# Optimization experiments

Hardware: AMD Instinct MI355X
Metric: run time of the kernel (lower is better)

The kernel has to match this reference:

```python
import jax, jax.numpy as jnp
import numpy as np

D = 2048  # input_size
H = 2048  # hidden_size
K = 4096  # number of children


def setup_inputs() -> dict:
    key = jax.random.key(0)
    ks = jax.random.split(key, 12)
    sD = 1.0 / np.sqrt(D)
    sH = 1.0 / np.sqrt(H)
    return {
        "input": jax.random.normal(ks[0], (D,), dtype=jnp.float32),
        "children_c": jax.random.normal(ks[1], (K, H), dtype=jnp.float32),
        "children_h": jax.random.normal(ks[2], (K, H), dtype=jnp.float32),
        "W_iou_x": jax.random.uniform(ks[3], (3 * H, D), jnp.float32, -sD, sD),
        "b_iou_x": jax.random.uniform(ks[4], (3 * H,), jnp.float32, -sD, sD),
        "W_iou_h": jax.random.uniform(ks[5], (3 * H, H), jnp.float32, -sH, sH),
        "b_iou_h": jax.random.uniform(ks[6], (3 * H,), jnp.float32, -sH, sH),
        "W_fx": jax.random.uniform(ks[7], (H, D), jnp.float32, -sD, sD),
        "b_fx": jax.random.uniform(ks[8], (H,), jnp.float32, -sD, sD),
        "W_fh": jax.random.uniform(ks[9], (H, H), jnp.float32, -sH, sH),
        "b_fh": jax.random.uniform(ks[10], (H,), jnp.float32, -sH, sH),
    }


def reference(input, children_c, children_h,
              W_iou_x, b_iou_x, W_iou_h, b_iou_h,
              W_fx, b_fx, W_fh, b_fh):
    # iou = iou_x(input) + iou_h(sum_k h_k)  -> [3H]
    h_sum = jnp.sum(children_h, axis=0)
    iou = (W_iou_x @ input + b_iou_x) + (W_iou_h @ h_sum + b_iou_h)
    i, o, u = jnp.split(iou, 3)
    i = jax.nn.sigmoid(i)
    o = jax.nn.sigmoid(o)
    u = jnp.tanh(u)
    # per-child forget gates, batched over K (original loops in Python):
    # f_k = sigmoid(f_x(input) + f_h(h_k))  -> [K, H]
    fx = W_fx @ input + b_fx                       # [H], computed once
    fh = children_h @ W_fh.T + b_fh                # [K, H] GEMM
    f = jax.nn.sigmoid(fx[None, :] + fh)           # [K, H]
    c = i * u + jnp.sum(f * children_c, axis=0)    # [H]
    h = o * jnp.tanh(c)                            # [H]
    return (o, c, h)
```

## Files before the change

### kernel.cpp

```cpp
#include <hip/hip_runtime.h>

typedef unsigned short u16;
typedef short bf16x8 __attribute__((ext_vector_type(8)));
typedef float f32x4 __attribute__((ext_vector_type(4)));

#define D_IN 2048
#define H_DIM 2048
#define K_CH 4096

__device__ __forceinline__ u16 f2bf(float f) {
  unsigned int u = __float_as_uint(f);
  u += 0x7fffu + ((u >> 16) & 1u);
  return (u16)(u >> 16);
}
__device__ __forceinline__ float sigmoidf(float x) {
  return 1.0f / (1.0f + __expf(-x));
}
__device__ __forceinline__ uint4 packrow(float4 a, float4 b) {
  uint4 w;
  w.x = (unsigned)f2bf(a.x) | ((unsigned)f2bf(a.y) << 16);
  w.y = (unsigned)f2bf(a.z) | ((unsigned)f2bf(a.w) << 16);
  w.z = (unsigned)f2bf(b.x) | ((unsigned)f2bf(b.y) << 16);
  w.w = (unsigned)f2bf(b.z) | ((unsigned)f2bf(b.w) << 16);
  return w;
}

__global__ __launch_bounds__(256) void k1(
    const float* __restrict__ ch, const float* __restrict__ wfh,
    const float* __restrict__ Wfx, const float* __restrict__ bfx,
    const float* __restrict__ bfh, const float* __restrict__ x,
    const float* __restrict__ Wix, const float* __restrict__ bix,
    const float* __restrict__ bih, float* __restrict__ partials,
    u16* __restrict__ chb, u16* __restrict__ wfhb, float* __restrict__ g,
    float* __restrict__ ioux, float* __restrict__ hsum,
    float* __restrict__ accv) {
  const int t = threadIdx.x;
  const int bid = blockIdx.x;
  if (bid < 1024) {
    const int r0 = bid * 4;
    float4 a[4], b[4];
#pragma unroll
    for (int r = 0; r < 4; ++r) {
      const float4* p = (const float4*)(ch + (size_t)(r0 + r) * H_DIM + t * 8);
      a[r] = p[0];
      b[r] = p[1];
    }
    float s0 = 0.f, s1 = 0.f, s2 = 0.f, s3 = 0.f;
    float s4 = 0.f, s5 = 0.f, s6 = 0.f, s7 = 0.f;
#pragma unroll
    for (int r = 0; r < 4; ++r) {
      s0 += a[r].x; s1 += a[r].y; s2 += a[r].z; s3 += a[r].w;
      s4 += b[r].x; s5 += b[r].y; s6 += b[r].z; s7 += b[r].w;
      *(uint4*)(chb + (size_t)(r0 + r) * H_DIM + t * 8) = packrow(a[r], b[r]);
    }
    float4 lo, hi;
    lo.x = s0; lo.y = s1; lo.z = s2; lo.w = s3;
    hi.x = s4; hi.y = s5; hi.z = s6; hi.w = s7;
    float* pp = partials + (size_t)bid * H_DIM + t * 8;
    *(float4*)pp = lo;
    *(float4*)(pp + 4) = hi;
  } else if (bid < 1536) {
    const size_t base = (size_t)(bid - 1024) * 8192 + t * 8;
    float4 a[4], b[4];
#pragma unroll
    for (int j = 0; j < 4; ++j) {
      const float4* p = (const float4*)(wfh + base + j * 2048);
      a[j] = p[0];
      b[j] = p[1];
    }
#pragma unroll
    for (int j = 0; j < 4; ++j)
      *(uint4*)(wfhb + base + j * 2048) = packrow(a[j], b[j]);
  } else if (bid < 2048) {
    const int wave = t >> 6, lane = t & 63;
    const int h = (bid - 1536) * 4 + wave;
    const float4* w = (const float4*)(Wfx + (size_t)h * D_IN);
    const float4* xv = (const float4*)x;
    float s = 0.f;
#pragma unroll
    for (int i = 0; i < 8; ++i) {
      int idx = i * 64 + lane;
      float4 av = w[idx], bv = xv[idx];
      s += av.x * bv.x + av.y * bv.y + av.z * bv.z + av.w * bv.w;
    }
#pragma unroll
    for (int off = 32; off > 0; off >>= 1) s += __shfl_xor(s, off);
    if (lane == 0) g[h] = s + bfx[h] + bfh[h];
  } else if (bid < 3584) {
    const int wave = t >> 6, lane = t & 63;
    const int row = (bid - 2048) * 4 + wave;
    const float4* w = (const float4*)(Wix + (size_t)row * D_IN);
    const float4* xv = (const float4*)x;
    float s = 0.f;
#pragma unroll
    for (int i = 0; i < 8; ++i) {
      int idx = i * 64 + lane;
      float4 av = w[idx], bv = xv[idx];
      s += av.x * bv.x + av.y * bv.y + av.z * bv.z + av.w * bv.w;
    }
#pragma unroll
    for (int off = 32; off > 0; off >>= 1) s += __shfl_xor(s, off);
    if (lane == 0) ioux[row] = s + bix[row] + bih[row];
  } else {
    float4 z = {0.f, 0.f, 0.f, 0.f};
    ((float4*)hsum)[t * 2] = z;
    ((float4*)hsum)[t * 2 + 1] = z;
    ((float4*)accv)[t * 2] = z;
    ((float4*)accv)[t * 2 + 1] = z;
  }
}

#define BM 256
#define BN 128
#define BK 64

__global__ __launch_bounds__(512) void kG(
    const u16* __restrict__ chb, const float* __restrict__ cc,
    const u16* __restrict__ wfhb, const float* __restrict__ g,
    const float* __restrict__ partials, float* __restrict__ hsum,
    float* __restrict__ accv) {
  __shared__ u16 As[3][BM * BK];
  __shared__ u16 Bs[3][BN * BK];

  const int bid = blockIdx.x;
  const int t = threadIdx.x;

  if (bid < 64) {
    const int c = (bid & 7) * 256 + (t & 255);
    const int p0 = (bid >> 3) * 128 + (t >> 8) * 64;
    float a0 = 0.f, a1 = 0.f, a2 = 0.f, a3 = 0.f;
    float a4 = 0.f, a5 = 0.f, a6 = 0.f, a7 = 0.f;
    for (int p = p0; p < p0 + 64; p += 8) {
      a0 += partials[(size_t)(p + 0) * H_DIM + c];
      a1 += partials[(size_t)(p + 1) * H_DIM + c];
      a2 += partials[(size_t)(p + 2) * H_DIM + c];
      a3 += partials[(size_t)(p + 3) * H_DIM + c];
      a4 += partials[(size_t)(p + 4) * H_DIM + c];
      a5 += partials[(size_t)(p + 5) * H_DIM + c];
      a6 += partials[(size_t)(p + 6) * H_DIM + c];
      a7 += partials[(size_t)(p + 7) * H_DIM + c];
    }
    float s = ((a0 + a1) + (a2 + a3)) + ((a4 + a5) + (a6 + a7));
    atomicAdd(hsum + c, s);
    return;
  }

  const int gb = bid - 64;
  const int xcd = gb & 7;
  const int u = gb >> 3;
  const int bm = (xcd << 1) | (u >> 4);
  const int bn = u & 15;
  const int row0 = bm * BM;
  const int col0 = bn * BN;

  const int wave = t >> 6, lane = t & 63;
  const int lrow = lane & 15, lquad = lane >> 4;
  const int wm = wave >> 1, wn = wave & 1;

  f32x4 acc[4][4] = {};
  bf16x8 faA[2][4], fbA[2][4];
  bf16x8 faB[2][4], fbB[2][4];

  const int srow = lane >> 3;
  const int schunk = (lane & 7) ^ srow;
  const u16* agbase = chb  + (size_t)(row0 + wave * 32 + srow) * H_DIM + schunk * 8;
  const u16* bgbase = wfhb + (size_t)(col0 + wave * 16 + srow) * H_DIM + schunk * 8;

#define STAGE(bi, kb)                                                         \
  do {                                                                        \
    _Pragma("unroll")                                                         \
    for (int i = 0; i < 4; ++i)                                               \
      __builtin_amdgcn_global_load_lds(                                       \
          (const __attribute__((address_space(1))) void*)(agbase + (size_t)i * 8 * H_DIM + (size_t)(kb) * BK), \
          (__attribute__((address_space(3))) void*)(&As[bi][(wave * 32 + i * 8) * 64]), \
          16, 0, 0);                                                          \
    _Pragma("unroll")                                                         \
    for (int i = 0; i < 2; ++i)                                               \
      __builtin_amdgcn_global_load_lds(                                       \
          (const __attribute__((address_space(1))) void*)(bgbase + (size_t)i * 8 * H_DIM + (size_t)(kb) * BK), \
          (__attribute__((address_space(3))) void*)(&Bs[bi][(wave * 16 + i * 8) * 64]), \
          16, 0, 0);                                                          \
  } while (0)

#define READ_SET(fax, fbx, bi)                                                \
  do {                                                                        \
    _Pragma("unroll")                                                         \
    for (int step = 0; step < 2; ++step) {                                    \
      const int slot = ((step * 4 + lquad) ^ (lrow & 7)) * 8;                 \
      _Pragma("unroll")                                                       \
      for (int i = 0; i < 4; ++i)                                             \
        fax[step][i] = *(const bf16x8*)(&As[bi][(wm * 64 + i * 16 + lrow) * 64 + slot]); \
      _Pragma("unroll")                                                       \
      for (int i = 0; i < 4; ++i)                                             \
        fbx[step][i] = *(const bf16x8*)(&Bs[bi][(wn * 64 + i * 16 + lrow) * 64 + slot]); \
    }                                                                         \
  } while (0)

#define COMPUTE_SET(fax, fbx)                                                 \
  do {                                                                        \
    __builtin_amdgcn_s_setprio(1);                                            \
    _Pragma("unroll")                                                         \
    for (int step = 0; step < 2; ++step)                                      \
      _Pragma("unroll")                                                       \
      for (int mi = 0; mi < 4; ++mi)                                          \
        _Pragma("unroll")                                                     \
        for (int ni = 0; ni < 4; ++ni)                                        \
          acc[mi][ni] = __builtin_amdgcn_mfma_f32_16x16x32_bf16(              \
              fax[step][mi], fbx[step][ni], acc[mi][ni], 0, 0, 0);            \
    __builtin_amdgcn_s_setprio(0);                                            \
  } while (0)

#define VMCNT6() do { asm volatile("s_waitcnt vmcnt(6)" ::: "memory");        \
                      __builtin_amdgcn_sched_barrier(0); } while (0)
#define VMCNT0() do { asm volatile("s_waitcnt vmcnt(0)" ::: "memory");        \
                      __builtin_amdgcn_sched_barrier(0); } while (0)
#define LGKM15() do { asm volatile("s_waitcnt lgkmcnt(15)" ::: "memory");     \
                      __builtin_amdgcn_sched_barrier(0); } while (0)
#define LGKM0()  do { asm volatile("s_waitcnt lgkmcnt(0)" ::: "memory");      \
                      __builtin_amdgcn_sched_barrier(0); } while (0)
#define SBAR()   do { __builtin_amdgcn_s_barrier();                           \
                      __builtin_amdgcn_sched_barrier(0); } while (0)

  STAGE(0, 0);
  STAGE(1, 1);
  VMCNT6();
  SBAR();
  READ_SET(faA, fbA, 0);

  int c0 = 0, c1 = 1, c2 = 2;
  for (int kb = 0; kb < 30; kb += 2) {
    STAGE(c2, kb + 2);
    VMCNT6();
    SBAR();
    READ_SET(faB, fbB, c1);
    LGKM15();
    COMPUTE_SET(faA, fbA);
    SBAR();
    STAGE(c0, kb + 3);
    VMCNT6();
    SBAR();
    READ_SET(faA, fbA, c2);
    LGKM15();
    COMPUTE_SET(faB, fbB);
    SBAR();
    const int tmp = c0; c0 = c2; c2 = c1; c1 = tmp;
  }
  VMCNT0();
  SBAR();
  READ_SET(faB, fbB, 1);
  LGKM15();
  COMPUTE_SET(faA, fbA);
  LGKM0();
  COMPUTE_SET(faB, fbB);

#pragma unroll
  for (int ni = 0; ni < 4; ++ni) {
    const int colg = col0 + wn * 64 + ni * 16 + lrow;
    const float gv = g[colg];
    float s = 0.f;
#pragma unroll
    for (int mi = 0; mi < 4; ++mi) {
      const int rowg = row0 + wm * 64 + mi * 16 + lquad * 4;
#pragma unroll
      for (int r = 0; r < 4; ++r) {
        float f = sigmoidf(gv + acc[mi][ni][r]);
        s += f * cc[(size_t)(rowg + r) * H_DIM + colg];
      }
    }
    s += __shfl_xor(s, 16);
    s += __shfl_xor(s, 32);
    if (lquad == 0) atomicAdd(accv + colg, s);
  }
#undef STAGE
#undef READ_SET
#undef COMPUTE_SET
#undef VMCNT6
#undef VMCNT0
#undef LGKM15
#undef LGKM0
#undef SBAR
}

__global__ __launch_bounds__(256) void kmvF(const float* __restrict__ Wih,
                                            const float* __restrict__ hsum,
                                            const float* __restrict__ ioux,
                                            const float* __restrict__ accv,
                                            float* __restrict__ out) {
  const int wave = threadIdx.x >> 6, lane = threadIdx.x & 63;
  const int h = blockIdx.x * 4 + wave;
  const float4* w0 = (const float4*)(Wih + (size_t)h * H_DIM);
  const float4* w1 = (const float4*)(Wih + (size_t)(H_DIM + h) * H_DIM);
  const float4* w2 = (const float4*)(Wih + (size_t)(2 * H_DIM + h) * H_DIM);
  const float4* hv = (const float4*)hsum;
  float s0 = 0.f, s1 = 0.f, s2 = 0.f;
#pragma unroll
  for (int i = 0; i < 8; ++i) {
    int idx = i * 64 + lane;
    float4 b = hv[idx];
    float4 a0 = w0[idx], a1 = w1[idx], a2 = w2[idx];
    s0 += a0.x * b.x + a0.y * b.y + a0.z * b.z + a0.w * b.w;
    s1 += a1.x * b.x + a1.y * b.y + a1.z * b.z + a1.w * b.w;
    s2 += a2.x * b.x + a2.y * b.y + a2.z * b.z + a2.w * b.w;
  }
#pragma unroll
  for (int off = 32; off > 0; off >>= 1) {
    s0 += __shfl_xor(s0, off);
    s1 += __shfl_xor(s1, off);
    s2 += __shfl_xor(s2, off);
  }
  if (lane == 0) {
    float i_ = sigmoidf(ioux[h] + s0);
    float o_ = sigmoidf(ioux[H_DIM + h] + s1);
    float u_ = tanhf(ioux[2 * H_DIM + h] + s2);
    float c_ = i_ * u_ + accv[h];
    float hh = o_ * tanhf(c_);
    out[h] = o_;
    out[H_DIM + h] = c_;
    out[2 * H_DIM + h] = hh;
  }
}

extern "C" void kernel_launch(void* const* d_in, const int* in_sizes, int n_in,
                              void* d_out, int out_size, void* d_ws, size_t ws_size,
                              hipStream_t stream) {
  const float* x   = (const float*)d_in[0];
  const float* cc  = (const float*)d_in[1];
  const float* ch  = (const float*)d_in[2];
  const float* Wix = (const float*)d_in[3];
  const float* bix = (const float*)d_in[4];
  const float* Wih = (const float*)d_in[5];
  const float* bih = (const float*)d_in[6];
  const float* Wfx = (const float*)d_in[7];
  const float* bfx = (const float*)d_in[8];
  const float* Wfh = (const float*)d_in[9];
  const float* bfh = (const float*)d_in[10];

  float* ws   = (float*)d_ws;
  float* hsum = ws;
  float* ioux = ws + 2048;
  float* g    = ws + 8192;
  float* accv = ws + 10240;
  float* partials = ws + 12288;
  u16* chb  = (u16*)(ws + 12288 + 1024 * 2048);
  u16* wfhb = chb + (size_t)K_CH * H_DIM;
  float* out = (float*)d_out;

  k1<<<3585, 256, 0, stream>>>(ch, Wfh, Wfx, bfx, bfh, x, Wix, bix, bih,
                               partials, chb, wfhb, g, ioux, hsum, accv);
  kG<<<320, 512, 0, stream>>>(chb, cc, wfhb, g, partials, hsum, accv);
  kmvF<<<512, 256, 0, stream>>>(Wih, hsum, ioux, accv, out);
}
```

Measured before the change: 256.0 us.

## Restructure GEMM main loop into four-phase interleaved LDS-read/MFMA schedule

```diff
diff --git a/kernel.cpp b/kernel.cpp
--- a/kernel.cpp
+++ b/kernel.cpp
@@ -158,22 +158,39 @@
   const int wm = wave >> 1, wn = wave & 1;
 
   f32x4 acc[4][4] = {};
-  bf16x8 faA[2][4], fbA[2][4];
-  bf16x8 faB[2][4], fbB[2][4];
+  bf16x8 fa0[4], fb0[4], fa1[4], fb1[4];
 
   const int srow = lane >> 3;
   const int schunk = (lane & 7) ^ srow;
   const u16* agbase = chb  + (size_t)(row0 + wave * 32 + srow) * H_DIM + schunk * 8;
   const u16* bgbase = wfhb + (size_t)(col0 + wave * 16 + srow) * H_DIM + schunk * 8;
 
-#define STAGE(bi, kb)                                                         \
+  const int slot0 = ((lquad) ^ (lrow & 7)) * 8;
+  const int slot1 = ((4 + lquad) ^ (lrow & 7)) * 8;
+  const int arow0 = (wm * 64 + 0 * 16 + lrow) * 64;
+  const int arow1 = (wm * 64 + 1 * 16 + lrow) * 64;
+  const int arow2 = (wm * 64 + 2 * 16 + lrow) * 64;
+  const int arow3 = (wm * 64 + 3 * 16 + lrow) * 64;
+  const int brow0 = (wn * 64 + 0 * 16 + lrow) * 64;
+  const int brow1 = (wn * 64 + 1 * 16 + lrow) * 64;
+  const int brow2 = (wn * 64 + 2 * 16 + lrow) * 64;
+  const int brow3 = (wn * 64 + 3 * 16 + lrow) * 64;
+
+#define LDA(bi, roff, sl) (*(const bf16x8*)(&As[bi][(roff) + (sl)]))
+#define LDB(bi, roff, sl) (*(const bf16x8*)(&Bs[bi][(roff) + (sl)]))
+
+#define STAGE_A2(bi, kb, i0)                                                  \
   do {                                                                        \
     _Pragma("unroll")                                                         \
-    for (int i = 0; i < 4; ++i)                                               \
+    for (int i = (i0); i < (i0) + 2; ++i)                                     \
       __builtin_amdgcn_global_load_lds(                                       \
           (const __attribute__((address_space(1))) void*)(agbase + (size_t)i * 8 * H_DIM + (size_t)(kb) * BK), \
           (__attribute__((address_space(3))) void*)(&As[bi][(wave * 32 + i * 8) * 64]), \
           16, 0, 0);                                                          \
+  } while (0)
+
+#define STAGE_B2(bi, kb)                                                      \
+  do {                                                                        \
     _Pragma("unroll")                                                         \
     for (int i = 0; i < 2; ++i)                                               \
       __builtin_amdgcn_global_load_lds(                                       \
@@ -182,76 +199,72 @@
           16, 0, 0);                                                          \
   } while (0)
 
-#define READ_SET(fax, fbx, bi)                                                \
-  do {                                                                        \
-    _Pragma("unroll")                                                         \
-    for (int step = 0; step < 2; ++step) {                                    \
-      const int slot = ((step * 4 + lquad) ^ (lrow & 7)) * 8;                 \
-      _Pragma("unroll")                                                       \
-      for (int i = 0; i < 4; ++i)                                             \
-        fax[step][i] = *(const bf16x8*)(&As[bi][(wm * 64 + i * 16 + lrow) * 64 + slot]); \
-      _Pragma("unroll")                                                       \
-      for (int i = 0; i < 4; ++i)                                             \
-        fbx[step][i] = *(const bf16x8*)(&Bs[bi][(wn * 64 + i * 16 + lrow) * 64 + slot]); \
-    }                                                                         \
-  } while (0)
-
-#define COMPUTE_SET(fax, fbx)                                                 \
+#define MFMA_HALF(fa, fb, M0)                                                 \
   do {                                                                        \
     __builtin_amdgcn_s_setprio(1);                                            \
     _Pragma("unroll")                                                         \
-    for (int step = 0; step < 2; ++step)                                      \
+    for (int mi = (M0); mi < (M0) + 2; ++mi)                                  \
       _Pragma("unroll")                                                       \
-      for (int mi = 0; mi < 4; ++mi)                                          \
-        _Pragma("unroll")                                                     \
-        for (int ni = 0; ni < 4; ++ni)                                        \
-          acc[mi][ni] = __builtin_amdgcn_mfma_f32_16x16x32_bf16(              \
-              fax[step][mi], fbx[step][ni], acc[mi][ni], 0, 0, 0);            \
+      for (int ni = 0; ni < 4; ++ni)                                          \
+        acc[mi][ni] = __builtin_amdgcn_mfma_f32_16x16x32_bf16(                \
+            fa[mi], fb[ni], acc[mi][ni], 0, 0, 0);                            \
     __builtin_amdgcn_s_setprio(0);                                            \
   } while (0)
 
 #define VMCNT6() do { asm volatile("s_waitcnt vmcnt(6)" ::: "memory");        \
                       __builtin_amdgcn_sched_barrier(0); } while (0)
 #define VMCNT0() do { asm volatile("s_waitcnt vmcnt(0)" ::: "memory");        \
-                      __builtin_amdgcn_sched_barrier(0); } while (0)
-#define LGKM15() do { asm volatile("s_waitcnt lgkmcnt(15)" ::: "memory");     \
                       __builtin_amdgcn_sched_barrier(0); } while (0)
 #define LGKM0()  do { asm volatile("s_waitcnt lgkmcnt(0)" ::: "memory");      \
                       __builtin_amdgcn_sched_barrier(0); } while (0)
 #define SBAR()   do { __builtin_amdgcn_s_barrier();                           \
                       __builtin_amdgcn_sched_barrier(0); } while (0)
 
-  STAGE(0, 0);
-  STAGE(1, 1);
+#define TILE(bufv, doStage, kb2, endvm)                                       \
+  do {                                                                        \
+                                \
+    fa0[0] = LDA(bufv, arow0, slot0); fa0[1] = LDA(bufv, arow1, slot0);       \
+    fb0[0] = LDB(bufv, brow0, slot0); fb0[1] = LDB(bufv, brow1, slot0);       \
+    fb0[2] = LDB(bufv, brow2, slot0); fb0[3] = LDB(bufv, brow3, slot0);       \
+    if (doStage) STAGE_A2(c2, kb2, 0);                                        \
+    SBAR(); LGKM0();                                                          \
+    MFMA_HALF(fa0, fb0, 0);                                                   \
+    SBAR();                                                                   \
+                                              \
+    fa0[2] = LDA(bufv, arow2, slot0); fa0[3] = LDA(bufv, arow3, slot0);       \
+    if (doStage) STAGE_A2(c2, kb2, 2);                                        \
+    SBAR(); LGKM0();                                                          \
+    MFMA_HALF(fa0, fb0, 2);                                                   \
+    SBAR();                                                                   \
+                                \
+    fa1[0] = LDA(bufv, arow0, slot1); fa1[1] = LDA(bufv, arow1, slot1);       \
+    fb1[0] = LDB(bufv, brow0, slot1); fb1[1] = LDB(bufv, brow1, slot1);       \
+    fb1[2] = LDB(bufv, brow2, slot1); fb1[3] = LDB(bufv, brow3, slot1);       \
+    if (doStage) STAGE_B2(c2, kb2);                                           \
+    SBAR(); LGKM0();                                                          \
+    MFMA_HALF(fa1, fb1, 0);                                                   \
+    SBAR();                                                                   \
+                              \
+    fa1[2] = LDA(bufv, arow2, slot1); fa1[3] = LDA(bufv, arow3, slot1);       \
+    SBAR(); LGKM0();                                                          \
+    MFMA_HALF(fa1, fb1, 2);                                                   \
+    if ((endvm) == 6) VMCNT6();                                               \
+    if ((endvm) == 0) VMCNT0();                                               \
+    if ((endvm) >= 0) SBAR();                                                 \
+  } while (0)
+
+  STAGE_A2(0, 0, 0); STAGE_A2(0, 0, 2); STAGE_B2(0, 0);
+  STAGE_A2(1, 1, 0); STAGE_A2(1, 1, 2); STAGE_B2(1, 1);
   VMCNT6();
   SBAR();
-  READ_SET(faA, fbA, 0);
 
   int c0 = 0, c1 = 1, c2 = 2;
-  for (int kb = 0; kb < 30; kb += 2) {
-    STAGE(c2, kb + 2);
-    VMCNT6();
-    SBAR();
-    READ_SET(faB, fbB, c1);
-    LGKM15();
-    COMPUTE_SET(faA, fbA);
-    SBAR();
-    STAGE(c0, kb + 3);
-    VMCNT6();
-    SBAR();
-    READ_SET(faA, fbA, c2);
-    LGKM15();
-    COMPUTE_SET(faB, fbB);
-    SBAR();
-    const int tmp = c0; c0 = c2; c2 = c1; c1 = tmp;
-  }
-  VMCNT0();
-  SBAR();
-  READ_SET(faB, fbB, 1);
-  LGKM15();
-  COMPUTE_SET(faA, fbA);
-  LGKM0();
-  COMPUTE_SET(faB, fbB);
+  for (int tt = 0; tt < 30; ++tt) {
+    TILE(c0, 1, tt + 2, 6);
+    const int tmp = c0; c0 = c1; c1 = c2; c2 = tmp;
+  }
+  TILE(c0, 0, 0, 0);
+  TILE(c1, 0, 0, -1);
 
 #pragma unroll
   for (int ni = 0; ni < 4; ++ni) {
@@ -271,14 +284,16 @@
     s += __shfl_xor(s, 32);
     if (lquad == 0) atomicAdd(accv + colg, s);
   }
-#undef STAGE
-#undef READ_SET
-#undef COMPUTE_SET
+#undef LDA
+#undef LDB
+#undef STAGE_A2
+#undef STAGE_B2
+#undef MFMA_HALF
 #undef VMCNT6
 #undef VMCNT0
-#undef LGKM15
 #undef LGKM0
 #undef SBAR
+#undef TILE
 }
 
 __global__ __launch_bounds__(256) void kmvF(const float* __restrict__ Wih,
```

New measurement: 264.0 us. 1.03x slower.
